# Kernel tuning notes

Measured on AMD Instinct MI355X. Metric: run time of the kernel, lower is better.

The kernel has to match this reference:

```python
import jax, jax.numpy as jnp
import numpy as np

N_CAT, IN, H, OUT = 1024, 1024, 2048, 32000


def _lstm_cell(x, h, c, w_ih, w_hh, b_ih, b_hh):
    # x: [1, D], h/c: [1, H]; PyTorch gate order: i, f, g, o
    gates = x @ w_ih.T + b_ih + h @ w_hh.T + b_hh  # [1, 4H]
    i, f, g, o = jnp.split(gates, 4, axis=-1)
    i = jax.nn.sigmoid(i)
    f = jax.nn.sigmoid(f)
    g = jnp.tanh(g)
    o = jax.nn.sigmoid(o)
    c_new = f * c + i * g
    h_new = o * jnp.tanh(c_new)
    return h_new, c_new


def setup_inputs() -> dict:
    key = jax.random.key(0)
    ks = jax.random.split(key, 16)
    s = 0.02
    return {
        "category": jax.random.normal(ks[0], (1, N_CAT), jnp.float32),
        "input": jax.random.normal(ks[1], (1, IN), jnp.float32),
        "hidden": jax.random.normal(ks[2], (2, 1, H), jnp.float32),
        "cell_state": jax.random.normal(ks[3], (2, 1, H), jnp.float32),
        # LSTM layer 0: input dim = N_CAT + IN
        "w_ih_l0": jax.random.normal(ks[4], (4 * H, N_CAT + IN), jnp.float32) * s,
        "w_hh_l0": jax.random.normal(ks[5], (4 * H, H), jnp.float32) * s,
        "b_ih_l0": jax.random.normal(ks[6], (4 * H,), jnp.float32) * s,
        "b_hh_l0": jax.random.normal(ks[7], (4 * H,), jnp.float32) * s,
        # LSTM layer 1: input dim = H
        "w_ih_l1": jax.random.normal(ks[8], (4 * H, H), jnp.float32) * s,
        "w_hh_l1": jax.random.normal(ks[9], (4 * H, H), jnp.float32) * s,
        "b_ih_l1": jax.random.normal(ks[10], (4 * H,), jnp.float32) * s,
        "b_hh_l1": jax.random.normal(ks[11], (4 * H,), jnp.float32) * s,
        # output linear: [OUT, N_CAT + H]
        "w_out": jax.random.normal(ks[12], (OUT, N_CAT + H), jnp.float32) * s,
        "b_out": jax.random.normal(ks[13], (OUT,), jnp.float32) * s,
    }


def reference(category, input, hidden, cell_state,
              w_ih_l0, w_hh_l0, b_ih_l0, b_hh_l0,
              w_ih_l1, w_hh_l1, b_ih_l1, b_hh_l1,
              w_out, b_out):
    # single-step, batch=1, seq=1; dropout layers are identity (eval mode)
    x = jnp.concatenate([category, input], axis=-1)  # [1, N_CAT+IN]
    h1, c1 = _lstm_cell(x, hidden[0], cell_state[0], w_ih_l0, w_hh_l0, b_ih_l0, b_hh_l0)
    h2, c2 = _lstm_cell(h1, hidden[1], cell_state[1], w_ih_l1, w_hh_l1, b_ih_l1, b_hh_l1)
    out_comb = jnp.concatenate([category, h2], axis=-1)  # [1, N_CAT+H]
    logits = out_comb @ w_out.T + b_out  # [1, OUT]
    logp = jax.nn.log_softmax(logits, axis=1)
    new_hidden = jnp.stack([h1, h2], axis=0)      # [2, 1, H]
    new_cell = jnp.stack([c1, c2], axis=0)        # [2, 1, H]
    return logp, new_hidden, new_cell
```

## Files before the change

kernel.cpp:

```cpp
#include <hip/hip_runtime.h>
#include <math.h>

#define HDIM 2048
#define OUTN 32000
#define KOUT 3072
#define NPART 1000

__device__ __forceinline__ float wave_reduce_sum(float v) {
    #pragma unroll
    for (int off = 32; off > 0; off >>= 1)
        v += __shfl_down(v, off, 64);
    return v;
}

__device__ __forceinline__ float dot4(float4 a, float4 b) {
    return a.x * b.x + a.y * b.y + a.z * b.z + a.w * b.w;
}

typedef float nfloat4 __attribute__((ext_vector_type(4)));
__device__ __forceinline__ float4 ldnt4(const float4* p) {
    nfloat4 v = __builtin_nontemporal_load((const nfloat4*)p);
    return make_float4(v.x, v.y, v.z, v.w);
}

__device__ __forceinline__ float sigmoidf_(float x) {
    return 1.0f / (1.0f + __expf(-x));
}

__global__ __launch_bounds__(256) void lstm_gemv(
    const float* __restrict__ xa,
    const float* __restrict__ xb,
    const float* __restrict__ h,
    const float* __restrict__ w_ih,
    const float* __restrict__ w_hh,
    const float* __restrict__ b_ih,
    const float* __restrict__ b_hh,
    float* __restrict__ gates)
{
    const int wave = threadIdx.x >> 6;
    const int lane = threadIdx.x & 63;
    const int g    = blockIdx.x * 4 + wave;
    const int r0   = g * 4;

    const float4* wi  = (const float4*)(w_ih + (size_t)r0 * HDIM);
    const float4* wh  = (const float4*)(w_hh + (size_t)r0 * HDIM);
    const float4* xa4 = (const float4*)xa;
    const float4* xb4 = (const float4*)xb;
    const float4* h4  = (const float4*)h;

    float a0 = 0.f, a1 = 0.f, a2 = 0.f, a3 = 0.f;
    #pragma unroll
    for (int it = 0; it < 8; ++it) {
        const int k4 = it * 64 + lane;
        float4 xv = (it < 4) ? xa4[k4] : xb4[k4 - 256];
        a0 += dot4(ldnt4(&wi[k4]),        xv);
        a1 += dot4(ldnt4(&wi[k4 + 512]),  xv);
        a2 += dot4(ldnt4(&wi[k4 + 1024]), xv);
        a3 += dot4(ldnt4(&wi[k4 + 1536]), xv);
    }
    #pragma unroll
    for (int it = 0; it < 8; ++it) {
        const int k4 = it * 64 + lane;
        float4 hv = h4[k4];
        a0 += dot4(ldnt4(&wh[k4]),        hv);
        a1 += dot4(ldnt4(&wh[k4 + 512]),  hv);
        a2 += dot4(ldnt4(&wh[k4 + 1024]), hv);
        a3 += dot4(ldnt4(&wh[k4 + 1536]), hv);
    }
    a0 = wave_reduce_sum(a0);
    a1 = wave_reduce_sum(a1);
    a2 = wave_reduce_sum(a2);
    a3 = wave_reduce_sum(a3);

    if (lane == 0) {
        float4 bi = ((const float4*)b_ih)[g];
        float4 bh = ((const float4*)b_hh)[g];
        ((float4*)gates)[g] = make_float4(a0 + bi.x + bh.x,
                                          a1 + bi.y + bh.y,
                                          a2 + bi.z + bh.z,
                                          a3 + bi.w + bh.w);
    }
}

__global__ __launch_bounds__(256) void lstm_point(
    const float* __restrict__ gates,
    const float* __restrict__ c,
    float* __restrict__ h_out,
    float* __restrict__ c_out)
{
    const int n = blockIdx.x * 256 + threadIdx.x;
    float gi = sigmoidf_(gates[n]);
    float gf = sigmoidf_(gates[HDIM + n]);
    float gg = tanhf(gates[2 * HDIM + n]);
    float go = sigmoidf_(gates[3 * HDIM + n]);
    float cn = gf * c[n] + gi * gg;
    float hn = go * tanhf(cn);
    c_out[n] = cn;
    h_out[n] = hn;
}

__global__ __launch_bounds__(256) void logits_kernel(
    const float* __restrict__ cat,
    const float* __restrict__ h2,
    const float* __restrict__ w_out,
    const float* __restrict__ b_out,
    float* __restrict__ logits,
    float2* __restrict__ partial)
{
    const int wave = threadIdx.x >> 6;
    const int lane = threadIdx.x & 63;
    const int row0 = blockIdx.x * 32 + wave * 8;

    const float4* w4 = (const float4*)(w_out + (size_t)row0 * KOUT);
    const float4* c4 = (const float4*)cat;
    const float4* h4 = (const float4*)h2;

    float a[8] = {0.f, 0.f, 0.f, 0.f, 0.f, 0.f, 0.f, 0.f};
    #pragma unroll
    for (int it = 0; it < 12; ++it) {
        const int k4 = it * 64 + lane;
        float4 v = (it < 4) ? c4[k4] : h4[k4 - 256];
        #pragma unroll
        for (int r = 0; r < 8; ++r)
            a[r] += dot4(ldnt4(&w4[k4 + r * 768]), v);
    }
    #pragma unroll
    for (int r = 0; r < 8; ++r)
        a[r] = wave_reduce_sum(a[r]);

    __shared__ float sm[4], ss[4];
    if (lane == 0) {
        #pragma unroll
        for (int r = 0; r < 8; ++r)
            a[r] += b_out[row0 + r];
        *(float4*)(logits + row0)     = make_float4(a[0], a[1], a[2], a[3]);
        *(float4*)(logits + row0 + 4) = make_float4(a[4], a[5], a[6], a[7]);
        float m = a[0];
        #pragma unroll
        for (int r = 1; r < 8; ++r) m = fmaxf(m, a[r]);
        float s = 0.f;
        #pragma unroll
        for (int r = 0; r < 8; ++r) s += __expf(a[r] - m);
        sm[wave] = m; ss[wave] = s;
    }
    __syncthreads();
    if (threadIdx.x == 0) {
        float M = sm[0], S = ss[0];
        #pragma unroll
        for (int w = 1; w < 4; ++w) {
            float mn = fmaxf(M, sm[w]);
            S = S * __expf(M - mn) + ss[w] * __expf(sm[w] - mn);
            M = mn;
        }
        partial[blockIdx.x] = make_float2(M, S);
    }
}

__global__ __launch_bounds__(256) void sub_fused(
    const float* __restrict__ logits,
    const float2* __restrict__ partial,
    float* __restrict__ out)
{
    float m = -INFINITY, s = 0.f;
    for (int i = threadIdx.x; i < NPART; i += 256) {
        float2 p  = partial[i];
        float  mn = fmaxf(m, p.x);
        s = s * __expf(m - mn) + p.y * __expf(p.x - mn);
        m = mn;
    }
    #pragma unroll
    for (int off = 32; off > 0; off >>= 1) {
        float m2 = __shfl_down(m, off, 64);
        float s2 = __shfl_down(s, off, 64);
        float mn = fmaxf(m, m2);
        s = s * __expf(m - mn) + s2 * __expf(m2 - mn);
        m = mn;
    }
    __shared__ float smm[4], sss[4], s_logz;
    const int wave = threadIdx.x >> 6;
    const int lane = threadIdx.x & 63;
    if (lane == 0) { smm[wave] = m; sss[wave] = s; }
    __syncthreads();
    if (threadIdx.x == 0) {
        float M = smm[0], S = sss[0];
        #pragma unroll
        for (int w = 1; w < 4; ++w) {
            float mn = fmaxf(M, smm[w]);
            S = S * __expf(M - mn) + sss[w] * __expf(smm[w] - mn);
            M = mn;
        }
        s_logz = M + logf(S);
    }
    __syncthreads();
    const int i = blockIdx.x * 256 + threadIdx.x;
    out[i] = logits[i] - s_logz;
}

extern "C" void kernel_launch(void* const* d_in, const int* in_sizes, int n_in,
                              void* d_out, int out_size, void* d_ws, size_t ws_size,
                              hipStream_t stream) {
    const float* category = (const float*)d_in[0];
    const float* input    = (const float*)d_in[1];
    const float* hidden   = (const float*)d_in[2];
    const float* cell     = (const float*)d_in[3];
    const float* w_ih_l0  = (const float*)d_in[4];
    const float* w_hh_l0  = (const float*)d_in[5];
    const float* b_ih_l0  = (const float*)d_in[6];
    const float* b_hh_l0  = (const float*)d_in[7];
    const float* w_ih_l1  = (const float*)d_in[8];
    const float* w_hh_l1  = (const float*)d_in[9];
    const float* b_ih_l1  = (const float*)d_in[10];
    const float* b_hh_l1  = (const float*)d_in[11];
    const float* w_out    = (const float*)d_in[12];
    const float* b_out    = (const float*)d_in[13];

    float* out  = (float*)d_out;
    float* logp = out;
    float* h1   = out + OUTN;
    float* h2   = out + OUTN + HDIM;
    float* c1   = out + OUTN + 2 * HDIM;
    float* c2   = out + OUTN + 3 * HDIM;

    float* gates    = (float*)d_ws;
    float* logits   = gates + 4 * HDIM;
    float2* partial = (float2*)(logits + OUTN);

    lstm_gemv<<<512, 256, 0, stream>>>(category, input, hidden,
                                       w_ih_l0, w_hh_l0, b_ih_l0, b_hh_l0,
                                       gates);
    lstm_point<<<8, 256, 0, stream>>>(gates, cell, h1, c1);
    lstm_gemv<<<512, 256, 0, stream>>>(h1, h1 + 1024, hidden + HDIM,
                                       w_ih_l1, w_hh_l1, b_ih_l1, b_hh_l1,
                                       gates);
    lstm_point<<<8, 256, 0, stream>>>(gates, cell + HDIM, h2, c2);

    logits_kernel<<<NPART, 256, 0, stream>>>(category, h2, w_out, b_out,
                                             logits, partial);
    sub_fused<<<OUTN / 256, 256, 0, stream>>>(logits, partial, logp);
}
```

Baseline: 652.1 us.

## Overlap category part of output projection with LSTM GEMV launches

Splits the output projection into a category part and an h2 part. The category part has no dependency on the LSTM, so it is computed by 500 extra blocks appended to each of the two LSTM GEMV launches, each covering half the rows. The final logits kernel then reads only the h2 columns and adds the stored partial sums. This moves a third of the w_out traffic off the serial tail so it runs alongside the memory-bound LSTM GEMVs, at the cost of an extra logits write and read and more contention within those launches.

```diff
diff --git a/kernel.cpp b/kernel.cpp
--- a/kernel.cpp
+++ b/kernel.cpp
@@ -27,7 +27,7 @@
     return 1.0f / (1.0f + __expf(-x));
 }
 
-__global__ __launch_bounds__(256) void lstm_gemv(
+__global__ __launch_bounds__(256) void lstm_cat_kernel(
     const float* __restrict__ xa,
     const float* __restrict__ xb,
     const float* __restrict__ h,
@@ -35,50 +35,81 @@
     const float* __restrict__ w_hh,
     const float* __restrict__ b_ih,
     const float* __restrict__ b_hh,
-    float* __restrict__ gates)
+    float* __restrict__ gates,
+    const float* __restrict__ cat,
+    const float* __restrict__ w_out,
+    float* __restrict__ logits,
+    int catRowBase)
 {
     const int wave = threadIdx.x >> 6;
     const int lane = threadIdx.x & 63;
-    const int g    = blockIdx.x * 4 + wave;
-    const int r0   = g * 4;
-
-    const float4* wi  = (const float4*)(w_ih + (size_t)r0 * HDIM);
-    const float4* wh  = (const float4*)(w_hh + (size_t)r0 * HDIM);
-    const float4* xa4 = (const float4*)xa;
-    const float4* xb4 = (const float4*)xb;
-    const float4* h4  = (const float4*)h;
-
-    float a0 = 0.f, a1 = 0.f, a2 = 0.f, a3 = 0.f;
-    #pragma unroll
-    for (int it = 0; it < 8; ++it) {
-        const int k4 = it * 64 + lane;
-        float4 xv = (it < 4) ? xa4[k4] : xb4[k4 - 256];
-        a0 += dot4(ldnt4(&wi[k4]),        xv);
-        a1 += dot4(ldnt4(&wi[k4 + 512]),  xv);
-        a2 += dot4(ldnt4(&wi[k4 + 1024]), xv);
-        a3 += dot4(ldnt4(&wi[k4 + 1536]), xv);
-    }
-    #pragma unroll
-    for (int it = 0; it < 8; ++it) {
-        const int k4 = it * 64 + lane;
-        float4 hv = h4[k4];
-        a0 += dot4(ldnt4(&wh[k4]),        hv);
-        a1 += dot4(ldnt4(&wh[k4 + 512]),  hv);
-        a2 += dot4(ldnt4(&wh[k4 + 1024]), hv);
-        a3 += dot4(ldnt4(&wh[k4 + 1536]), hv);
-    }
-    a0 = wave_reduce_sum(a0);
-    a1 = wave_reduce_sum(a1);
-    a2 = wave_reduce_sum(a2);
-    a3 = wave_reduce_sum(a3);
-
-    if (lane == 0) {
-        float4 bi = ((const float4*)b_ih)[g];
-        float4 bh = ((const float4*)b_hh)[g];
-        ((float4*)gates)[g] = make_float4(a0 + bi.x + bh.x,
-                                          a1 + bi.y + bh.y,
-                                          a2 + bi.z + bh.z,
-                                          a3 + bi.w + bh.w);
+
+    if (blockIdx.x < 512) {
+        const int g  = blockIdx.x * 4 + wave;
+        const int r0 = g * 4;
+
+        const float4* wi  = (const float4*)(w_ih + (size_t)r0 * HDIM);
+        const float4* wh  = (const float4*)(w_hh + (size_t)r0 * HDIM);
+        const float4* xa4 = (const float4*)xa;
+        const float4* xb4 = (const float4*)xb;
+        const float4* h4  = (const float4*)h;
+
+        float a0 = 0.f, a1 = 0.f, a2 = 0.f, a3 = 0.f;
+        #pragma unroll
+        for (int it = 0; it < 8; ++it) {
+            const int k4 = it * 64 + lane;
+            float4 xv = (it < 4) ? xa4[k4] : xb4[k4 - 256];
+            a0 += dot4(ldnt4(&wi[k4]),        xv);
+            a1 += dot4(ldnt4(&wi[k4 + 512]),  xv);
+            a2 += dot4(ldnt4(&wi[k4 + 1024]), xv);
+            a3 += dot4(ldnt4(&wi[k4 + 1536]), xv);
+        }
+        #pragma unroll
+        for (int it = 0; it < 8; ++it) {
+            const int k4 = it * 64 + lane;
+            float4 hv = h4[k4];
+            a0 += dot4(ldnt4(&wh[k4]),        hv);
+            a1 += dot4(ldnt4(&wh[k4 + 512]),  hv);
+            a2 += dot4(ldnt4(&wh[k4 + 1024]), hv);
+            a3 += dot4(ldnt4(&wh[k4 + 1536]), hv);
+        }
+        a0 = wave_reduce_sum(a0);
+        a1 = wave_reduce_sum(a1);
+        a2 = wave_reduce_sum(a2);
+        a3 = wave_reduce_sum(a3);
+
+        if (lane == 0) {
+            float4 bi = ((const float4*)b_ih)[g];
+            float4 bh = ((const float4*)b_hh)[g];
+            ((float4*)gates)[g] = make_float4(a0 + bi.x + bh.x,
+                                              a1 + bi.y + bh.y,
+                                              a2 + bi.z + bh.z,
+                                              a3 + bi.w + bh.w);
+        }
+    } else {
+        const int j    = blockIdx.x - 512;
+        const int row0 = catRowBase + j * 32 + wave * 8;
+
+        const float4* w4 = (const float4*)(w_out + (size_t)row0 * KOUT);
+        const float4* c4 = (const float4*)cat;
+
+        float a[8] = {0.f, 0.f, 0.f, 0.f, 0.f, 0.f, 0.f, 0.f};
+        #pragma unroll
+        for (int it = 0; it < 4; ++it) {
+            const int k4 = it * 64 + lane;
+            float4 v = c4[k4];
+            #pragma unroll
+            for (int r = 0; r < 8; ++r)
+                a[r] += dot4(ldnt4(&w4[k4 + r * 768]), v);
+        }
+        #pragma unroll
+        for (int r = 0; r < 8; ++r)
+            a[r] = wave_reduce_sum(a[r]);
+
+        if (lane == 0) {
+            *(float4*)(logits + row0)     = make_float4(a[0], a[1], a[2], a[3]);
+            *(float4*)(logits + row0 + 4) = make_float4(a[4], a[5], a[6], a[7]);
+        }
     }
 }
 
@@ -99,8 +130,7 @@
     h_out[n] = hn;
 }
 
-__global__ __launch_bounds__(256) void logits_kernel(
-    const float* __restrict__ cat,
+__global__ __launch_bounds__(256) void logits_h2_kernel(
     const float* __restrict__ h2,
     const float* __restrict__ w_out,
     const float* __restrict__ b_out,
@@ -111,15 +141,14 @@
     const int lane = threadIdx.x & 63;
     const int row0 = blockIdx.x * 32 + wave * 8;
 
-    const float4* w4 = (const float4*)(w_out + (size_t)row0 * KOUT);
-    const float4* c4 = (const float4*)cat;
+    const float4* w4 = (const float4*)(w_out + (size_t)row0 * KOUT + 1024);
     const float4* h4 = (const float4*)h2;
 
     float a[8] = {0.f, 0.f, 0.f, 0.f, 0.f, 0.f, 0.f, 0.f};
     #pragma unroll
-    for (int it = 0; it < 12; ++it) {
+    for (int it = 0; it < 8; ++it) {
         const int k4 = it * 64 + lane;
-        float4 v = (it < 4) ? c4[k4] : h4[k4 - 256];
+        float4 v = h4[k4];
         #pragma unroll
         for (int r = 0; r < 8; ++r)
             a[r] += dot4(ldnt4(&w4[k4 + r * 768]), v);
@@ -132,7 +161,7 @@
     if (lane == 0) {
         #pragma unroll
         for (int r = 0; r < 8; ++r)
-            a[r] += b_out[row0 + r];
+            a[r] += logits[row0 + r] + b_out[row0 + r];
         *(float4*)(logits + row0)     = make_float4(a[0], a[1], a[2], a[3]);
         *(float4*)(logits + row0 + 4) = make_float4(a[4], a[5], a[6], a[7]);
         float m = a[0];
@@ -225,16 +254,16 @@
     float* logits   = gates + 4 * HDIM;
     float2* partial = (float2*)(logits + OUTN);
 
-    lstm_gemv<<<512, 256, 0, stream>>>(category, input, hidden,
-                                       w_ih_l0, w_hh_l0, b_ih_l0, b_hh_l0,
-                                       gates);
+    lstm_cat_kernel<<<1012, 256, 0, stream>>>(category, input, hidden,
+                                              w_ih_l0, w_hh_l0, b_ih_l0, b_hh_l0,
+                                              gates, category, w_out, logits, 0);
     lstm_point<<<8, 256, 0, stream>>>(gates, cell, h1, c1);
-    lstm_gemv<<<512, 256, 0, stream>>>(h1, h1 + 1024, hidden + HDIM,
-                                       w_ih_l1, w_hh_l1, b_ih_l1, b_hh_l1,
-                                       gates);
+    lstm_cat_kernel<<<1012, 256, 0, stream>>>(h1, h1 + 1024, hidden + HDIM,
+                                              w_ih_l1, w_hh_l1, b_ih_l1, b_hh_l1,
+                                              gates, category, w_out, logits, 16000);
     lstm_point<<<8, 256, 0, stream>>>(gates, cell + HDIM, h2, c2);
 
-    logits_kernel<<<NPART, 256, 0, stream>>>(category, h2, w_out, b_out,
-                                             logits, partial);
+    logits_h2_kernel<<<NPART, 256, 0, stream>>>(h2, w_out, b_out,
+                                                logits, partial);
     sub_fused<<<OUTN / 256, 256, 0, stream>>>(logits, partial, logp);
 }
```

New measurement: 655.5 us. About the same (+0.5%).
